# Performance work log

Measured on AMD Instinct MI355X. Metric: run time of the kernel, lower is better.

## Reference

```python
import jax, jax.numpy as jnp
import numpy as np

MAX_LAG = 24
SEASONAL_LAGS = [12, 24]
EPS = 1e-8


def setup_inputs() -> dict:
    key = jax.random.key(0)
    k1, k2, k3, k4 = jax.random.split(key, 4)
    B, T, F, D = 128, 8192, 8, 256
    input_sequence = jax.random.normal(k1, (B, T, F), dtype=jnp.float32)
    hidden_states = jax.random.normal(k2, (B, T, D), dtype=jnp.float32)
    # torch init is ones; add small noise so softmax/grads are non-degenerate
    lag_weights = 1.0 + 0.1 * jax.random.normal(k3, (MAX_LAG,), dtype=jnp.float32)
    seasonal_importance = 1.0 + 0.1 * jax.random.normal(k4, (len(SEASONAL_LAGS),), dtype=jnp.float32)
    return {
        "input_sequence": input_sequence,
        "hidden_states": hidden_states,
        "lag_weights": lag_weights,
        "seasonal_importance": seasonal_importance,
    }


def _pearson(x, y):
    # x, y: [B, N] -> [B]; matches torch.corrcoef off-diagonal (clipped to [-1,1])
    xm = x - x.mean(axis=1, keepdims=True)
    ym = y - y.mean(axis=1, keepdims=True)
    num = (xm * ym).sum(axis=1)
    den = jnp.sqrt((xm * xm).sum(axis=1)) * jnp.sqrt((ym * ym).sum(axis=1))
    return jnp.clip(num / den, -1.0, 1.0)


def reference(input_sequence, hidden_states, lag_weights, seasonal_importance):
    seq = input_sequence[:, :, 0]                      # [B, T] claims channel
    T = seq.shape[1]
    mean = seq.mean(axis=1, keepdims=True)
    std = seq.std(axis=1, ddof=1, keepdims=True)       # torch .std() is unbiased
    seqn = (seq - mean) / (std + EPS)                  # [B, T]

    n_lags = min(MAX_LAG, T - 1)
    # vectorized over batch; small fixed Python loop over lags (<=24)
    autocorr = jnp.stack(
        [_pearson(seqn[:, :-lag], seqn[:, lag:]) for lag in range(1, n_lags + 1)],
        axis=1,
    )                                                  # [B, n_lags]

    w = jax.nn.softmax(lag_weights[:n_lags])           # [n_lags]
    weighted = (autocorr * w).sum(axis=1)              # [B]

    seasonal = jnp.zeros_like(weighted)
    for i, lag in enumerate(SEASONAL_LAGS):
        if lag <= n_lags:
            seasonal = seasonal + autocorr[:, lag - 1] * seasonal_importance[i]

    return (weighted + seasonal).mean()
```

## Files before the change

kernel.cpp:

```cpp
#include <hip/hip_runtime.h>
#include <math.h>

#define T_LEN 8192
#define N_B   128
#define N_F   8
#define NLAGS 24
#define EPSN  1e-8

__device__ __forceinline__ double wred(double v) {
    #pragma unroll
    for (int o = 32; o > 0; o >>= 1) v += __shfl_down(v, o, 64);
    return v;
}

__global__ __launch_bounds__(256)
void autocorr_batch_kernel(const float* __restrict__ seq,
                           const float* __restrict__ lw,
                           const float* __restrict__ si,
                           double* __restrict__ ws) {
    __shared__ float  sn[T_LEN];
    __shared__ double s4[2][4];
    __shared__ double sxy[NLAGS][4];
    __shared__ double sbc[2];

    const int b    = blockIdx.x;
    const int tid  = threadIdx.x;
    const int wave = tid >> 6;
    const int lane = tid & 63;
    const size_t base = (size_t)b * T_LEN * N_F;

    float r[32];
    double s = 0.0, q = 0.0;
    #pragma unroll
    for (int i = 0; i < 32; i++) {
        int t = i * 256 + tid;
        float v = seq[base + (size_t)t * N_F];
        r[i] = v;
        s += v;
        q += (double)v * (double)v;
    }
    s = wred(s); q = wred(q);
    if (lane == 0) { s4[0][wave] = s; s4[1][wave] = q; }
    __syncthreads();
    if (tid == 0) {
        double S = s4[0][0] + s4[0][1] + s4[0][2] + s4[0][3];
        double Q = s4[1][0] + s4[1][1] + s4[1][2] + s4[1][3];
        double mean = S / (double)T_LEN;
        double var  = (Q - S * S / (double)T_LEN) / (double)(T_LEN - 1);
        sbc[0] = mean;
        sbc[1] = 1.0 / (sqrt(var) + EPSN);
    }
    __syncthreads();
    const double mean = sbc[0];
    const double inv  = sbc[1];

    s = 0.0; q = 0.0;
    #pragma unroll
    for (int i = 0; i < 32; i++) {
        float f = (float)(((double)r[i] - mean) * inv);
        r[i] = f;
        sn[i * 256 + tid] = f;
        s += f;
        q += (double)f * (double)f;
    }
    s = wred(s); q = wred(q);
    if (lane == 0) { s4[0][wave] = s; s4[1][wave] = q; }
    __syncthreads();

    double S_all = 0.0, Q_all = 0.0;
    if (tid == 0) {
        S_all = s4[0][0] + s4[0][1] + s4[0][2] + s4[0][3];
        Q_all = s4[1][0] + s4[1][1] + s4[1][2] + s4[1][3];
    }

    #pragma unroll 1
    for (int lag = 1; lag <= NLAGS; lag++) {
        double acc = 0.0;
        #pragma unroll
        for (int i = 0; i < 32; i++) {
            int t = i * 256 + tid;
            if (t < T_LEN - lag)
                acc += (double)r[i] * (double)sn[t + lag];
        }
        acc = wred(acc);
        if (lane == 0) sxy[lag - 1][wave] = acc;
    }
    __syncthreads();

    if (tid == 0) {
        double m = -1e300;
        for (int l = 0; l < NLAGS; l++) { double x = (double)lw[l]; if (x > m) m = x; }
        double wsum = 0.0;
        for (int l = 0; l < NLAGS; l++) wsum += exp((double)lw[l] - m);

        double pre_s = 0.0, pre_q = 0.0, suf_s = 0.0, suf_q = 0.0, v = 0.0;
        for (int lag = 1; lag <= NLAGS; lag++) {
            float fp = sn[lag - 1];
            float fs = sn[T_LEN - lag];
            pre_s += fp; pre_q += (double)fp * (double)fp;
            suf_s += fs; suf_q += (double)fs * (double)fs;
            double n  = (double)(T_LEN - lag);
            double sx = S_all - suf_s;
            double sy = S_all - pre_s;
            double qx = Q_all - suf_q;
            double qy = Q_all - pre_q;
            double xy = sxy[lag - 1][0] + sxy[lag - 1][1] + sxy[lag - 1][2] + sxy[lag - 1][3];
            double num = xy - sx * sy / n;
            double dx  = qx - sx * sx / n;
            double dy  = qy - sy * sy / n;
            double den = sqrt(dx) * sqrt(dy);
            double rr  = num / den;
            rr = fmin(1.0, fmax(-1.0, rr));
            double wgt = exp((double)lw[lag - 1] - m) / wsum;
            v += rr * wgt;
            if (lag == 12) v += rr * (double)si[0];
            if (lag == 24) v += rr * (double)si[1];
        }
        ws[b] = v;
    }
}

__global__ __launch_bounds__(64)
void final_reduce_kernel(const double* __restrict__ ws, float* __restrict__ out) {
    int tid = threadIdx.x;
    double v = ws[tid] + ws[tid + 64];
    v = wred(v);
    if (tid == 0) out[0] = (float)(v / (double)N_B);
}

extern "C" void kernel_launch(void* const* d_in, const int* in_sizes, int n_in,
                              void* d_out, int out_size, void* d_ws, size_t ws_size,
                              hipStream_t stream) {
    const float* seq = (const float*)d_in[0];
    const float* lw  = (const float*)d_in[2];
    const float* si  = (const float*)d_in[3];
    float* out = (float*)d_out;
    double* ws = (double*)d_ws;

    autocorr_batch_kernel<<<N_B, 256, 0, stream>>>(seq, lw, si, ws);
    final_reduce_kernel<<<1, 64, 0, stream>>>(ws, out);
}
```

Before: 1.162 ms.

## Split each series into chunks and compute raw lag partial sums in parallel

Each batch row is split into 8 chunks handled by separate blocks, which compute raw lagged cross-products and sums directly from the unnormalized input. This relies on Pearson correlation being invariant to the mean/std normalization, so that pass is dropped. A second small kernel combines the chunk partials and applies the boundary corrections and softmax weighting per lag. The aim is to occupy far more compute units and avoid the serial per-lag loop. The cost is an extra launch, a workspace round trip, and slightly different floating-point rounding from skipping normalization.

```diff
diff --git a/kernel.cpp b/kernel.cpp
--- a/kernel.cpp
+++ b/kernel.cpp
@@ -5,7 +5,9 @@
 #define N_B   128
 #define N_F   8
 #define NLAGS 24
-#define EPSN  1e-8
+#define CHUNK 1024
+#define NCHK  8
+#define NPART 26
 
 __device__ __forceinline__ double wred(double v) {
     #pragma unroll
@@ -14,116 +16,126 @@
 }
 
 __global__ __launch_bounds__(256)
-void autocorr_batch_kernel(const float* __restrict__ seq,
-                           const float* __restrict__ lw,
-                           const float* __restrict__ si,
-                           double* __restrict__ ws) {
-    __shared__ float  sn[T_LEN];
-    __shared__ double s4[2][4];
-    __shared__ double sxy[NLAGS][4];
-    __shared__ double sbc[2];
+void partials_kernel(const float* __restrict__ seq, double* __restrict__ part) {
+    __shared__ float  sx[CHUNK + NLAGS];
+    __shared__ double sp[4][NPART];
 
-    const int b    = blockIdx.x;
+    const int bc = blockIdx.x;
+    const int b  = bc >> 3;
+    const int c  = bc & 7;
+    const int t0 = c * CHUNK;
     const int tid  = threadIdx.x;
     const int wave = tid >> 6;
     const int lane = tid & 63;
     const size_t base = (size_t)b * T_LEN * N_F;
 
-    float r[32];
-    double s = 0.0, q = 0.0;
-    #pragma unroll
-    for (int i = 0; i < 32; i++) {
-        int t = i * 256 + tid;
-        float v = seq[base + (size_t)t * N_F];
-        r[i] = v;
-        s += v;
-        q += (double)v * (double)v;
-    }
-    s = wred(s); q = wred(q);
-    if (lane == 0) { s4[0][wave] = s; s4[1][wave] = q; }
-    __syncthreads();
-    if (tid == 0) {
-        double S = s4[0][0] + s4[0][1] + s4[0][2] + s4[0][3];
-        double Q = s4[1][0] + s4[1][1] + s4[1][2] + s4[1][3];
-        double mean = S / (double)T_LEN;
-        double var  = (Q - S * S / (double)T_LEN) / (double)(T_LEN - 1);
-        sbc[0] = mean;
-        sbc[1] = 1.0 / (sqrt(var) + EPSN);
-    }
-    __syncthreads();
-    const double mean = sbc[0];
-    const double inv  = sbc[1];
-
-    s = 0.0; q = 0.0;
-    #pragma unroll
-    for (int i = 0; i < 32; i++) {
-        float f = (float)(((double)r[i] - mean) * inv);
-        r[i] = f;
-        sn[i * 256 + tid] = f;
-        s += f;
-        q += (double)f * (double)f;
-    }
-    s = wred(s); q = wred(q);
-    if (lane == 0) { s4[0][wave] = s; s4[1][wave] = q; }
-    __syncthreads();
-
-    double S_all = 0.0, Q_all = 0.0;
-    if (tid == 0) {
-        S_all = s4[0][0] + s4[0][1] + s4[0][2] + s4[0][3];
-        Q_all = s4[1][0] + s4[1][1] + s4[1][2] + s4[1][3];
-    }
-
-    #pragma unroll 1
-    for (int lag = 1; lag <= NLAGS; lag++) {
-        double acc = 0.0;
-        #pragma unroll
-        for (int i = 0; i < 32; i++) {
-            int t = i * 256 + tid;
-            if (t < T_LEN - lag)
-                acc += (double)r[i] * (double)sn[t + lag];
-        }
-        acc = wred(acc);
-        if (lane == 0) sxy[lag - 1][wave] = acc;
+    for (int idx = tid; idx < CHUNK + NLAGS; idx += 256) {
+        int t = t0 + idx;
+        sx[idx] = (t < T_LEN) ? seq[base + (size_t)t * N_F] : 0.0f;
     }
     __syncthreads();
 
-    if (tid == 0) {
-        double m = -1e300;
-        for (int l = 0; l < NLAGS; l++) { double x = (double)lw[l]; if (x > m) m = x; }
-        double wsum = 0.0;
-        for (int l = 0; l < NLAGS; l++) wsum += exp((double)lw[l] - m);
+    const int tl = tid * 4;
+    float r[4 + NLAGS];
+    #pragma unroll
+    for (int j = 0; j < 4 + NLAGS; j++) r[j] = sx[tl + j];
 
-        double pre_s = 0.0, pre_q = 0.0, suf_s = 0.0, suf_q = 0.0, v = 0.0;
-        for (int lag = 1; lag <= NLAGS; lag++) {
-            float fp = sn[lag - 1];
-            float fs = sn[T_LEN - lag];
-            pre_s += fp; pre_q += (double)fp * (double)fp;
-            suf_s += fs; suf_q += (double)fs * (double)fs;
-            double n  = (double)(T_LEN - lag);
-            double sx = S_all - suf_s;
-            double sy = S_all - pre_s;
-            double qx = Q_all - suf_q;
-            double qy = Q_all - pre_q;
-            double xy = sxy[lag - 1][0] + sxy[lag - 1][1] + sxy[lag - 1][2] + sxy[lag - 1][3];
-            double num = xy - sx * sy / n;
-            double dx  = qx - sx * sx / n;
-            double dy  = qy - sy * sy / n;
-            double den = sqrt(dx) * sqrt(dy);
-            double rr  = num / den;
-            rr = fmin(1.0, fmax(-1.0, rr));
-            double wgt = exp((double)lw[lag - 1] - m) / wsum;
-            v += rr * wgt;
-            if (lag == 12) v += rr * (double)si[0];
-            if (lag == 24) v += rr * (double)si[1];
-        }
-        ws[b] = v;
+    double s = 0.0, q = 0.0;
+    #pragma unroll
+    for (int j = 0; j < 4; j++) { double v = r[j]; s += v; q += v * v; }
+
+    double xy[NLAGS];
+    #pragma unroll
+    for (int l = 0; l < NLAGS; l++) {
+        double a = 0.0;
+        #pragma unroll
+        for (int j = 0; j < 4; j++) a += (double)r[j] * (double)r[j + l + 1];
+        xy[l] = a;
+    }
+
+    #pragma unroll
+    for (int k = 0; k < NLAGS; k++) {
+        double v = wred(xy[k]);
+        if (lane == 0) sp[wave][k] = v;
+    }
+    {
+        double v = wred(s);
+        if (lane == 0) sp[wave][24] = v;
+        v = wred(q);
+        if (lane == 0) sp[wave][25] = v;
+    }
+    __syncthreads();
+    if (tid < NPART) {
+        part[(size_t)bc * NPART + tid] =
+            sp[0][tid] + sp[1][tid] + sp[2][tid] + sp[3][tid];
     }
 }
 
 __global__ __launch_bounds__(64)
-void final_reduce_kernel(const double* __restrict__ ws, float* __restrict__ out) {
+void pearson_kernel(const double* __restrict__ part,
+                    const float* __restrict__ seq,
+                    const float* __restrict__ lw,
+                    const float* __restrict__ si,
+                    double* __restrict__ ws2) {
+    __shared__ double red[NPART];
+    __shared__ float  bnd[2][NLAGS];
+
+    const int b = blockIdx.x;
+    const int l = threadIdx.x;
+    const size_t base = (size_t)b * T_LEN * N_F;
+
+    if (l < NPART) {
+        double a = 0.0;
+        for (int c = 0; c < NCHK; c++)
+            a += part[(size_t)((b << 3) + c) * NPART + l];
+        red[l] = a;
+    }
+    if (l < NLAGS) {
+        bnd[0][l] = seq[base + (size_t)l * N_F];
+        bnd[1][l] = seq[base + (size_t)(T_LEN - 1 - l) * N_F];
+    }
+    __syncthreads();
+
+    double contrib = 0.0;
+    if (l < NLAGS) {
+        const int lag = l + 1;
+        const double S = red[24], Q = red[25];
+        double ps = 0.0, pq = 0.0, ss = 0.0, sq = 0.0;
+        for (int j = 0; j < lag; j++) {
+            double xp = bnd[0][j], xs = bnd[1][j];
+            ps += xp; pq += xp * xp;
+            ss += xs; sq += xs * xs;
+        }
+        const double n  = (double)(T_LEN - lag);
+        const double sx = S - ss;
+        const double sy = S - ps;
+        const double qx = Q - sq;
+        const double qy = Q - pq;
+        const double xy = red[l];
+        const double num = xy - sx * sy / n;
+        const double dx  = qx - sx * sx / n;
+        const double dy  = qy - sy * sy / n;
+        double r = num / (sqrt(dx) * sqrt(dy));
+        r = fmin(1.0, fmax(-1.0, r));
+
+        double m = -1e300;
+        for (int k = 0; k < NLAGS; k++) m = fmax(m, (double)lw[k]);
+        double wsum = 0.0;
+        for (int k = 0; k < NLAGS; k++) wsum += exp((double)lw[k] - m);
+        const double w = exp((double)lw[l] - m) / wsum;
+
+        contrib = r * w;
+        if (lag == 12) contrib += r * (double)si[0];
+        if (lag == 24) contrib += r * (double)si[1];
+    }
+    contrib = wred(contrib);
+    if (l == 0) ws2[b] = contrib;
+}
+
+__global__ __launch_bounds__(64)
+void final_reduce_kernel(const double* __restrict__ ws2, float* __restrict__ out) {
     int tid = threadIdx.x;
-    double v = ws[tid] + ws[tid + 64];
+    double v = ws2[tid] + ws2[tid + 64];
     v = wred(v);
     if (tid == 0) out[0] = (float)(v / (double)N_B);
 }
@@ -135,8 +147,11 @@
     const float* lw  = (const float*)d_in[2];
     const float* si  = (const float*)d_in[3];
     float* out = (float*)d_out;
-    double* ws = (double*)d_ws;
 
-    autocorr_batch_kernel<<<N_B, 256, 0, stream>>>(seq, lw, si, ws);
-    final_reduce_kernel<<<1, 64, 0, stream>>>(ws, out);
+    double* part = (double*)d_ws;
+    double* ws2  = part + (size_t)N_B * NCHK * NPART;
+
+    partials_kernel<<<N_B * NCHK, 256, 0, stream>>>(seq, part);
+    pearson_kernel<<<N_B, 64, 0, stream>>>(part, seq, lw, si, ws2);
+    final_reduce_kernel<<<1, 64, 0, stream>>>(ws2, out);
 }
```

New measurement: 1.151 ms. Within noise of the previous version (-0.9%).
